# Kernel optimization log

Measured on AMD Instinct MI355X. Metric: run time of the kernel, lower is better.

The kernel has to match this reference:

```python
import jax, jax.numpy as jnp
import numpy as np

DELTA_V = 0.1
DELTA_D = 0.5
NUM_LABELS = 33  # label 0 = background, instance ids 1..32


def setup_inputs() -> dict:
    key = jax.random.key(0)
    k1, k2 = jax.random.split(key)
    B, N, D = 8, 131072, 32
    embeddings = jax.random.normal(k1, (B, N, D), dtype=jnp.float32)
    labels = jax.random.randint(k2, (B, N), 0, NUM_LABELS, dtype=jnp.int32)
    return {"embeddings": embeddings, "labels": labels}


def reference(embeddings, labels):
    # embeddings: [B, N, D], labels: [B, N] int (0 = ignore)
    B = embeddings.shape[0]
    dt = embeddings.dtype

    oh = jax.nn.one_hot(labels, NUM_LABELS, dtype=dt)              # [B, N, L]
    counts = oh.sum(1)                                              # [B, L]
    sums = jnp.einsum('bnl,bnd->bld', oh, embeddings)               # [B, L, D]
    means = sums / jnp.maximum(counts, 1.0)[..., None]              # [B, L, D]

    # ---- pull loss: hinge on distance of each point to its instance mean ----
    mean_pt = jnp.take_along_axis(means, labels[..., None], axis=1)  # [B, N, D]
    diff = embeddings - mean_pt
    dist = jnp.sqrt(jnp.sum(diff * diff, -1) + 1e-24)               # [B, N]
    hinge = jnp.maximum(dist - DELTA_V, 0.0)
    seg_mean = jnp.einsum('bnl,bn->bl', oh, hinge) / jnp.maximum(counts, 1.0)  # [B, L]

    present = counts[:, 1:] > 0                                     # [B, L-1]
    n_inst = present.sum(-1).astype(dt)                             # [B]
    pull_b = seg_mean[:, 1:].sum(-1) / (n_inst + 1e-6)
    pull = pull_b.sum() / B

    # ---- push loss: hinge margin between normalized instance means ----
    m = means[:, 1:, :]                                             # [B, L-1, D]
    mn = m / jnp.maximum(jnp.linalg.norm(m, axis=-1, keepdims=True), 1e-12)
    sq = jnp.sum((mn[:, :, None, :] - mn[:, None, :, :]) ** 2, -1)  # [B, K, K]
    dmat = jnp.sqrt(sq + 1e-24)
    K = NUM_LABELS - 1
    triu = jnp.triu(jnp.ones((K, K), dt), 1)
    pmask = triu[None] * present[:, :, None].astype(dt) * present[:, None, :].astype(dt)
    hp = jnp.maximum(2.0 * DELTA_D - dmat, 0.0) * pmask
    push_b = jnp.where(n_inst > 1, hp.sum((-2, -1)) / (pmask.sum((-2, -1)) + 1e-6), 0.0)
    push = push_b.sum() / B

    total = pull + push
    return jnp.stack([total, pull, push])
```

## Files before the change

### kernel.cpp

```cpp
#include <hip/hip_runtime.h>
#include <hip/hip_bf16.h>

#define BATCH 8
#define NPTS  131072
#define DIM   32
#define NLAB  33
#define G1X   128
#define P1PTS 1024
#define BPB2  128

#define OFF_CNT   0
#define OFF_SUM   264
#define OFF_PULL  (264 + 8448)
#define OFF_PSUM  (OFF_PULL + BATCH * BPB2)
#define OFF_PCNT  (OFF_PSUM + BATCH * G1X * NLAB * DIM)
#define WS_FLOATS (OFF_PCNT + BATCH * G1X * NLAB)

typedef short  bf16x8 __attribute__((ext_vector_type(8)));
typedef float  f32x4  __attribute__((ext_vector_type(4)));
typedef float  f32x2  __attribute__((ext_vector_type(2)));
typedef int    i32x4  __attribute__((ext_vector_type(4)));

static __device__ __forceinline__ short f2bf(float f) {
  __hip_bfloat16 h = __float2bfloat16(f);
  return *reinterpret_cast<short*>(&h);
}

#define P1_WAIT(N)                                                            \
  asm volatile("s_waitcnt vmcnt(" #N ")" ::: "memory");                       \
  __builtin_amdgcn_sched_barrier(0);

#define P1_ISSUE(EV, L0, L1, T)                                               \
  {                                                                           \
    const int vt  = ve + (T) * 4096;                                          \
    const int vlt = vl + (T) * 128;                                           \
    asm volatile("global_load_dwordx4 %0, %1, %2"             : "=&v"(EV[0]) : "v"(vt),  "s"(ebase)); \
    asm volatile("global_load_dwordx4 %0, %1, %2 offset:1024" : "=&v"(EV[1]) : "v"(vt),  "s"(ebase)); \
    asm volatile("global_load_dwordx4 %0, %1, %2 offset:2048" : "=&v"(EV[2]) : "v"(vt),  "s"(ebase)); \
    asm volatile("global_load_dwordx4 %0, %1, %2 offset:3072" : "=&v"(EV[3]) : "v"(vt),  "s"(ebase)); \
    asm volatile("global_load_dwordx4 %0, %1, %2"             : "=&v"(L0)    : "v"(vlt), "s"(lbase)); \
    asm volatile("global_load_dwordx4 %0, %1, %2 offset:16"   : "=&v"(L1)    : "v"(vlt), "s"(lbase)); \
  }

#define P1_STAGE(EV, BUF)                                                     \
  {                                                                           \
    float* st_ = s_st[w][BUF];                                                \
    _Pragma("unroll")                                                         \
    for (int r = 0; r < 4; ++r) {                                             \
      const int idx = (r * 8 + (lane >> 3)) * 34 + (lane & 7) * 4;            \
      *(f32x2*)&st_[idx]     = (f32x2){EV[r][0], EV[r][1]};                   \
      *(f32x2*)&st_[idx + 2] = (f32x2){EV[r][2], EV[r][3]};                   \
    }                                                                         \
  }

#define P1_FRAGA(L0, L1)                                                      \
  {                                                                           \
    _Pragma("unroll")                                                         \
    for (int j = 0; j < 8; ++j) {                                             \
      const int lj = (j < 4) ? L0[j] : L1[j - 4];                             \
      const int h0 = (lj == m0), h1 = (lj == m0 + 16), h2 = (lj == m0 + 32);  \
      a0[j] = h0 ? (short)0x3F80 : (short)0;                                  \
      a1[j] = h1 ? (short)0x3F80 : (short)0;                                  \
      a2[j] = h2 ? (short)0x3F80 : (short)0;                                  \
      cnt0 += h0; cnt1 += h1; cnt2 += h2;                                     \
    }                                                                         \
  }

#define P1_BMFMA(BUF)                                                         \
  {                                                                           \
    const float* st_ = s_st[w][BUF];                                          \
    bf16x8 b0, b1;                                                            \
    _Pragma("unroll")                                                         \
    for (int j = 0; j < 8; ++j) {                                             \
      b0[j] = f2bf(st_[(g * 8 + j) * 34 + m0]);                               \
      b1[j] = f2bf(st_[(g * 8 + j) * 34 + m0 + 16]);                          \
    }                                                                         \
    acc[0][0] = __builtin_amdgcn_mfma_f32_16x16x32_bf16(a0, b0, acc[0][0], 0, 0, 0); \
    acc[0][1] = __builtin_amdgcn_mfma_f32_16x16x32_bf16(a0, b1, acc[0][1], 0, 0, 0); \
    acc[1][0] = __builtin_amdgcn_mfma_f32_16x16x32_bf16(a1, b0, acc[1][0], 0, 0, 0); \
    acc[1][1] = __builtin_amdgcn_mfma_f32_16x16x32_bf16(a1, b1, acc[1][1], 0, 0, 0); \
    acc[2][0] = __builtin_amdgcn_mfma_f32_16x16x32_bf16(a2, b0, acc[2][0], 0, 0, 0); \
    acc[2][1] = __builtin_amdgcn_mfma_f32_16x16x32_bf16(a2, b1, acc[2][1], 0, 0, 0); \
  }

__global__ __launch_bounds__(256) void pass1_kernel(
    const float* __restrict__ emb, const int* __restrict__ lab,
    float* __restrict__ psum, float* __restrict__ pcnt) {
  const int b    = blockIdx.y;
  const int tid  = threadIdx.x;
  const int w    = __builtin_amdgcn_readfirstlane(tid >> 6);
  const int lane = tid & 63;
  const int m0   = lane & 15;
  const int g    = lane >> 4;

  __shared__ float s_st[4][2][1088];
  __shared__ int   s_cnt4[4][NLAB];

  const size_t base = (size_t)b * NPTS + (size_t)blockIdx.x * P1PTS
                    + (size_t)w * 256;
  const float* ebase = emb + base * DIM;
  const int*   lbase = lab + base;
  const int ve = (lane >> 3) * 128 + (lane & 7) * 16;
  const int vl = g * 32;

  f32x4 acc[3][2];
#pragma unroll
  for (int t = 0; t < 3; ++t)
#pragma unroll
    for (int u = 0; u < 2; ++u) acc[t][u] = (f32x4){0.f, 0.f, 0.f, 0.f};
  int cnt0 = 0, cnt1 = 0, cnt2 = 0;
  bf16x8 a0, a1, a2;

  f32x4 eA[4], eB[4];
  i32x4 lA0, lA1, lB0, lB1;

  P1_ISSUE(eA, lA0, lA1, 0);
  P1_ISSUE(eB, lB0, lB1, 1);

  P1_WAIT(6); P1_STAGE(eA, 0); P1_FRAGA(lA0, lA1); P1_ISSUE(eA, lA0, lA1, 2); P1_BMFMA(0);
  P1_WAIT(6); P1_STAGE(eB, 1); P1_FRAGA(lB0, lB1); P1_ISSUE(eB, lB0, lB1, 3); P1_BMFMA(1);
  P1_WAIT(6); P1_STAGE(eA, 0); P1_FRAGA(lA0, lA1); P1_ISSUE(eA, lA0, lA1, 4); P1_BMFMA(0);
  P1_WAIT(6); P1_STAGE(eB, 1); P1_FRAGA(lB0, lB1); P1_ISSUE(eB, lB0, lB1, 5); P1_BMFMA(1);
  P1_WAIT(6); P1_STAGE(eA, 0); P1_FRAGA(lA0, lA1); P1_ISSUE(eA, lA0, lA1, 6); P1_BMFMA(0);
  P1_WAIT(6); P1_STAGE(eB, 1); P1_FRAGA(lB0, lB1); P1_ISSUE(eB, lB0, lB1, 7); P1_BMFMA(1);
  P1_WAIT(6); P1_STAGE(eA, 0); P1_FRAGA(lA0, lA1); P1_BMFMA(0);
  P1_WAIT(0); P1_STAGE(eB, 1); P1_FRAGA(lB0, lB1); P1_BMFMA(1);

  cnt0 += __shfl_xor(cnt0, 16); cnt0 += __shfl_xor(cnt0, 32);
  cnt1 += __shfl_xor(cnt1, 16); cnt1 += __shfl_xor(cnt1, 32);
  cnt2 += __shfl_xor(cnt2, 16); cnt2 += __shfl_xor(cnt2, 32);
  if (lane < 16)            s_cnt4[w][m0]      = cnt0;
  else if (lane < 32)       s_cnt4[w][m0 + 16] = cnt1;
  if (lane == 32)           s_cnt4[w][32]      = cnt2;

  float* st = &s_st[w][0][0];
#pragma unroll
  for (int t = 0; t < 2; ++t)
#pragma unroll
    for (int u = 0; u < 2; ++u)
#pragma unroll
      for (int r = 0; r < 4; ++r)
        st[(t * 16 + g * 4 + r) * DIM + m0 + 16 * u] = acc[t][u][r];
  if (lane < 16) {
    st[32 * DIM + m0]      = acc[2][0][0];
    st[32 * DIM + m0 + 16] = acc[2][1][0];
  }
  __syncthreads();

  const size_t pb = (size_t)b * G1X + blockIdx.x;
  for (int i = tid; i < NLAB * DIM; i += 256) {
    const float v = s_st[0][0][i] + s_st[1][0][i] + s_st[2][0][i] + s_st[3][0][i];
    psum[pb * (NLAB * DIM) + i] = v;
  }
  if (tid < NLAB) {
    const int c = s_cnt4[0][tid] + s_cnt4[1][tid] + s_cnt4[2][tid] + s_cnt4[3][tid];
    pcnt[pb * NLAB + tid] = (float)c;
  }
}

__global__ __launch_bounds__(256) void reduce_kernel(
    const float* __restrict__ psum, const float* __restrict__ pcnt,
    float* __restrict__ gsum, float* __restrict__ gcnt) {
  constexpr int TOT = BATCH * NLAB * DIM;
  constexpr int KS  = G1X / 8;
  const int slice = blockIdx.y;
  const int o = blockIdx.x * 256 + threadIdx.x;
  if (o < TOT) {
    const int b = o / (NLAB * DIM), i = o - b * (NLAB * DIM);
    const float* src = psum + ((size_t)b * G1X + slice * KS) * (NLAB * DIM) + i;
    float a0 = 0.f, a1 = 0.f, a2 = 0.f, a3 = 0.f;
#pragma unroll
    for (int k = 0; k < KS; k += 4) {
      a0 += src[(size_t)(k + 0) * (NLAB * DIM)];
      a1 += src[(size_t)(k + 1) * (NLAB * DIM)];
      a2 += src[(size_t)(k + 2) * (NLAB * DIM)];
      a3 += src[(size_t)(k + 3) * (NLAB * DIM)];
    }
    atomicAdd(&gsum[o], (a0 + a1) + (a2 + a3));
  } else if (o - TOT < BATCH * NLAB) {
    const int o2 = o - TOT;
    const int b = o2 / NLAB, l = o2 - b * NLAB;
    const float* src = pcnt + ((size_t)b * G1X + slice * KS) * NLAB + l;
    float a = 0.f;
#pragma unroll
    for (int k = 0; k < KS; ++k) a += src[(size_t)k * NLAB];
    atomicAdd(&gcnt[o2], a);
  }
}

#define CN 8
#define P2_ISSUE(LB, EB, C)                                                   \
  {                                                                           \
    _Pragma("unroll")                                                         \
    for (int j = 0; j < CN; ++j) {                                            \
      const size_t it = (size_t)(C) * CN + j;                                 \
      const unsigned long long al =                                           \
          (unsigned long long)(lab + base + p0 + it * PSTRIDE);               \
      asm volatile("global_load_dword %0, %1, off" : "=&v"(LB[j]) : "v"(al)); \
    }                                                                         \
    _Pragma("unroll")                                                         \
    for (int j = 0; j < CN; ++j) {                                            \
      const size_t it = (size_t)(C) * CN + j;                                 \
      const unsigned long long ae =                                           \
          (unsigned long long)(emb + (base + p0 + it * PSTRIDE) * DIM + d0);  \
      asm volatile("global_load_dwordx4 %0, %1, off" : "=&v"(EB[j]) : "v"(ae)); \
    }                                                                         \
  }

#define P2_COMPUTE(LB, EB)                                                    \
  {                                                                           \
    float s[CN];                                                              \
    _Pragma("unroll")                                                         \
    for (int j = 0; j < CN; ++j) {                                            \
      const f32x4 mv = *(const f32x4*)(s_mean + LB[j] * 36 + d0);             \
      const float dx = EB[j][0] - mv[0], dy = EB[j][1] - mv[1];               \
      const float dz = EB[j][2] - mv[2], dw = EB[j][3] - mv[3];               \
      s[j] = dx * dx + dy * dy + dz * dz + dw * dw;                           \
    }                                                                         \
    _Pragma("unroll")                                                         \
    for (int j = 0; j < CN; ++j) {                                            \
      s[j] += __shfl_xor(s[j], 1);                                            \
      s[j] += __shfl_xor(s[j], 2);                                            \
      s[j] += __shfl_xor(s[j], 4);                                            \
    }                                                                         \
    float sv = s[0];                                                          \
    int   lv = LB[0];                                                         \
    _Pragma("unroll")                                                         \
    for (int j = 1; j < CN; ++j) {                                            \
      sv = (lane8 == j) ? s[j] : sv;                                          \
      lv = (lane8 == j) ? LB[j] : lv;                                         \
    }                                                                         \
    const float dist = sqrtf(sv + 1e-24f);                                    \
    wacc += s_w[lv] * fmaxf(dist - 0.1f, 0.f);                                \
  }

__global__ __launch_bounds__(256, 4) void pass2_kernel(
    const float* __restrict__ emb, const int* __restrict__ lab,
    const float* __restrict__ gsum, const float* __restrict__ gcnt,
    float* __restrict__ pull_part) {
  const int b   = blockIdx.y;
  const int tid = threadIdx.x;
  __shared__ __align__(16) float s_mean[NLAB * 36];
  __shared__ float s_w[NLAB];
  __shared__ float s_red[4];

  for (int i = tid; i < NLAB * DIM; i += 256) {
    const int l = i >> 5, d = i & 31;
    const float c = gcnt[b * NLAB + l];
    s_mean[l * 36 + d] = gsum[b * (NLAB * DIM) + i] / fmaxf(c, 1.0f);
  }
  if (tid < 64) {
    const float c = (tid < NLAB) ? gcnt[b * NLAB + tid] : 0.f;
    const int pres = (tid >= 1 && tid < NLAB && c > 0.f) ? 1 : 0;
    const unsigned long long bal = __ballot(pres);
    const float n_inst = (float)__popcll(bal);
    if (tid < NLAB)
      s_w[tid] = pres ? 1.f / (fmaxf(c, 1.f) * (n_inst + 1e-6f)) : 0.f;
  }
  __syncthreads();

  const int sub   = tid >> 3;
  const int lane8 = tid & 7;
  const int d0    = lane8 << 2;
  const size_t base = (size_t)b * NPTS;
  const int p0 = blockIdx.x * 32 + sub;
  constexpr int PSTRIDE = BPB2 * 32;
  constexpr int NIT     = NPTS / PSTRIDE;
  constexpr int NCH     = NIT / CN;

  int   labsA[CN], labsB[CN];
  f32x4 eA[CN], eB[CN];
  float wacc = 0.f;

  P2_ISSUE(labsA, eA, 0);
#pragma unroll
  for (int cc = 0; cc < NCH; cc += 2) {
    if (cc + 1 < NCH) P2_ISSUE(labsB, eB, cc + 1);
    if (cc + 1 < NCH) { asm volatile("s_waitcnt vmcnt(16)" ::: "memory"); }
    else              { asm volatile("s_waitcnt vmcnt(0)"  ::: "memory"); }
    __builtin_amdgcn_sched_barrier(0);
    P2_COMPUTE(labsA, eA);
    if (cc + 1 < NCH) {
      if (cc + 2 < NCH) P2_ISSUE(labsA, eA, cc + 2);
      if (cc + 2 < NCH) { asm volatile("s_waitcnt vmcnt(16)" ::: "memory"); }
      else              { asm volatile("s_waitcnt vmcnt(0)"  ::: "memory"); }
      __builtin_amdgcn_sched_barrier(0);
      P2_COMPUTE(labsB, eB);
    }
  }

#pragma unroll
  for (int mm = 1; mm < 64; mm <<= 1) wacc += __shfl_xor(wacc, mm);
  if ((tid & 63) == 0) s_red[tid >> 6] = wacc;
  __syncthreads();
  if (tid == 0)
    pull_part[b * BPB2 + blockIdx.x] =
        s_red[0] + s_red[1] + s_red[2] + s_red[3];
}

__global__ __launch_bounds__(512) void finish_kernel(
    const float* __restrict__ gsum, const float* __restrict__ gcnt,
    const float* __restrict__ pull_part, float* __restrict__ out) {
  const int tid = threadIdx.x;
  const int b   = tid >> 6;
  const int t   = tid & 63;
  __shared__ __align__(16) float s_mn[BATCH * 32 * DIM];
  __shared__ float s_ps[BATCH];
  __shared__ float s_pl[BATCH];
  float* mn = s_mn + b * 32 * DIM;

  {
    float plsum = pull_part[b * BPB2 + t] + pull_part[b * BPB2 + 64 + t];
#pragma unroll
    for (int m = 1; m < 64; m <<= 1) plsum += __shfl_xor(plsum, m);
    if (t == 0) s_pl[b] = plsum;
  }

  int pres = 0;
  if (t < 32) {
    const int l = t + 1;
    const float cnt = gcnt[b * NLAB + l];
    pres = (cnt > 0.f) ? 1 : 0;
    const float inv = 1.f / fmaxf(cnt, 1.f);
    float v[DIM];
    float n2 = 0.f;
    for (int d = 0; d < DIM; d++) {
      v[d] = gsum[b * (NLAB * DIM) + l * DIM + d] * inv;
      n2  += v[d] * v[d];
    }
    const float scale = 1.f / fmaxf(sqrtf(n2), 1e-12f);
    for (int d = 0; d < DIM; d++) mn[t * DIM + d] = v[d] * scale;
  }
  const unsigned long long bal = __ballot(pres);
  const unsigned int pmask32 = (unsigned int)(bal & 0xFFFFFFFFull);
  const int n_inst = __popc(pmask32);

  __syncthreads();

  float hp_sum = 0.f, pm_sum = 0.f;
  for (int idx = t; idx < 1024; idx += 64) {
    const int i = idx >> 5, j = idx & 31;
    if (j > i && ((pmask32 >> i) & 1u) && ((pmask32 >> j) & 1u)) {
      const float4* a = (const float4*)(mn + i * DIM);
      const float4* c = (const float4*)(mn + j * DIM);
      float sq = 0.f;
      for (int q = 0; q < 8; q++) {
        const float4 av = a[q], cv = c[q];
        const float dx = av.x - cv.x, dy = av.y - cv.y;
        const float dz = av.z - cv.z, dw = av.w - cv.w;
        sq += dx * dx + dy * dy + dz * dz + dw * dw;
      }
      const float dmat = sqrtf(sq + 1e-24f);
      hp_sum += fmaxf(1.0f - dmat, 0.f);
      pm_sum += 1.f;
    }
  }
  for (int m = 1; m < 64; m <<= 1) {
    hp_sum += __shfl_xor(hp_sum, m);
    pm_sum += __shfl_xor(pm_sum, m);
  }
  const float push = (n_inst > 1) ? hp_sum / (pm_sum + 1e-6f) : 0.f;
  if (t == 0) s_ps[b] = push;
  __syncthreads();

  if (tid < 64) {
    float pl = (t < BATCH) ? s_pl[t] : 0.f;
    float ps = (t < BATCH) ? s_ps[t] : 0.f;
#pragma unroll
    for (int m = 1; m < 64; m <<= 1) {
      pl += __shfl_xor(pl, m);
      ps += __shfl_xor(ps, m);
    }
    if (t == 0) {
      const float pull_m = pl / (float)BATCH;
      const float push_m = ps / (float)BATCH;
      out[0] = pull_m + push_m;
      out[1] = pull_m;
      out[2] = push_m;
    }
  }
}

extern "C" void kernel_launch(void* const* d_in, const int* in_sizes, int n_in,
                              void* d_out, int out_size, void* d_ws, size_t ws_size,
                              hipStream_t stream) {
  const float* emb = (const float*)d_in[0];
  const int*   lab = (const int*)d_in[1];
  float* out = (float*)d_out;
  float* ws  = (float*)d_ws;

  float* gcnt  = ws + OFF_CNT;
  float* gsum  = ws + OFF_SUM;
  float* pullp = ws + OFF_PULL;
  float* psum  = ws + OFF_PSUM;
  float* pcnt  = ws + OFF_PCNT;

  hipMemsetAsync(d_ws, 0, (OFF_SUM + BATCH * NLAB * DIM) * sizeof(float), stream);

  dim3 grid1(G1X, BATCH);
  dim3 gridR((BATCH * NLAB * DIM + BATCH * NLAB + 255) / 256, 8);
  dim3 grid2(BPB2, BATCH);
  pass1_kernel<<<grid1, 256, 0, stream>>>(emb, lab, psum, pcnt);
  reduce_kernel<<<gridR, 256, 0, stream>>>(psum, pcnt, gsum, gcnt);
  pass2_kernel<<<grid2, 256, 0, stream>>>(emb, lab, gsum, gcnt, pullp);
  finish_kernel<<<1, 512, 0, stream>>>(gsum, gcnt, pullp, out);
}
```

Before: 233.8 us.

## Fold reduce and finish kernels into last-block-done tails of pass1 and pass2

Removes the separate reduce and finish kernel launches. Each pass1 block now bumps a per-batch atomic counter, and the last block for that batch reduces all partial sums and counts into gsum/gcnt. The last pass2 block across the grid computes the push loss and the final output. This saves two launches and their gaps, and the memset shrinks to a few counters. The cost is that the cross-block reduction is serialized onto one block per batch, which relies on threadfence/atomic ordering.

```diff
diff --git a/kernel.cpp b/kernel.cpp
--- a/kernel.cpp
+++ b/kernel.cpp
@@ -12,7 +12,8 @@
 #define OFF_CNT   0
 #define OFF_SUM   264
 #define OFF_PULL  (264 + 8448)
-#define OFF_PSUM  (OFF_PULL + BATCH * BPB2)
+#define OFF_DCNT  (OFF_PULL + BATCH * BPB2)
+#define OFF_PSUM  (OFF_DCNT + 16)
 #define OFF_PCNT  (OFF_PSUM + BATCH * G1X * NLAB * DIM)
 #define WS_FLOATS (OFF_PCNT + BATCH * G1X * NLAB)
 
@@ -85,7 +86,9 @@
 
 __global__ __launch_bounds__(256) void pass1_kernel(
     const float* __restrict__ emb, const int* __restrict__ lab,
-    float* __restrict__ psum, float* __restrict__ pcnt) {
+    float* __restrict__ psum, float* __restrict__ pcnt,
+    float* __restrict__ gsum, float* __restrict__ gcnt,
+    unsigned* __restrict__ dcnt) {
   const int b    = blockIdx.y;
   const int tid  = threadIdx.x;
   const int w    = __builtin_amdgcn_readfirstlane(tid >> 6);
@@ -95,6 +98,7 @@
 
   __shared__ float s_st[4][2][1088];
   __shared__ int   s_cnt4[4][NLAB];
+  __shared__ unsigned s_old;
 
   const size_t base = (size_t)b * NPTS + (size_t)blockIdx.x * P1PTS
                     + (size_t)w * 256;
@@ -156,35 +160,31 @@
     const int c = s_cnt4[0][tid] + s_cnt4[1][tid] + s_cnt4[2][tid] + s_cnt4[3][tid];
     pcnt[pb * NLAB + tid] = (float)c;
   }
-}
-
-__global__ __launch_bounds__(256) void reduce_kernel(
-    const float* __restrict__ psum, const float* __restrict__ pcnt,
-    float* __restrict__ gsum, float* __restrict__ gcnt) {
-  constexpr int TOT = BATCH * NLAB * DIM;
-  constexpr int KS  = G1X / 8;
-  const int slice = blockIdx.y;
-  const int o = blockIdx.x * 256 + threadIdx.x;
-  if (o < TOT) {
-    const int b = o / (NLAB * DIM), i = o - b * (NLAB * DIM);
-    const float* src = psum + ((size_t)b * G1X + slice * KS) * (NLAB * DIM) + i;
-    float a0 = 0.f, a1 = 0.f, a2 = 0.f, a3 = 0.f;
-#pragma unroll
-    for (int k = 0; k < KS; k += 4) {
-      a0 += src[(size_t)(k + 0) * (NLAB * DIM)];
-      a1 += src[(size_t)(k + 1) * (NLAB * DIM)];
-      a2 += src[(size_t)(k + 2) * (NLAB * DIM)];
-      a3 += src[(size_t)(k + 3) * (NLAB * DIM)];
+
+  __threadfence();
+  __syncthreads();
+  if (tid == 0) s_old = atomicAdd(&dcnt[b], 1u);
+  __syncthreads();
+  if (s_old == G1X - 1) {
+    for (int i = tid; i < NLAB * DIM; i += 256) {
+      const float* src = psum + (size_t)b * G1X * (NLAB * DIM) + i;
+      float r0 = 0.f, r1 = 0.f, r2 = 0.f, r3 = 0.f;
+#pragma unroll 4
+      for (int k = 0; k < G1X; k += 4) {
+        r0 += src[(size_t)(k + 0) * (NLAB * DIM)];
+        r1 += src[(size_t)(k + 1) * (NLAB * DIM)];
+        r2 += src[(size_t)(k + 2) * (NLAB * DIM)];
+        r3 += src[(size_t)(k + 3) * (NLAB * DIM)];
+      }
+      gsum[b * (NLAB * DIM) + i] = (r0 + r1) + (r2 + r3);
     }
-    atomicAdd(&gsum[o], (a0 + a1) + (a2 + a3));
-  } else if (o - TOT < BATCH * NLAB) {
-    const int o2 = o - TOT;
-    const int b = o2 / NLAB, l = o2 - b * NLAB;
-    const float* src = pcnt + ((size_t)b * G1X + slice * KS) * NLAB + l;
-    float a = 0.f;
-#pragma unroll
-    for (int k = 0; k < KS; ++k) a += src[(size_t)k * NLAB];
-    atomicAdd(&gcnt[o2], a);
+    for (int l = tid; l < NLAB; l += 256) {
+      const float* src = pcnt + (size_t)b * G1X * NLAB + l;
+      float r = 0.f;
+#pragma unroll 4
+      for (int k = 0; k < G1X; ++k) r += src[(size_t)k * NLAB];
+      gcnt[b * NLAB + l] = r;
+    }
   }
 }
 
@@ -237,12 +237,16 @@
 __global__ __launch_bounds__(256, 4) void pass2_kernel(
     const float* __restrict__ emb, const int* __restrict__ lab,
     const float* __restrict__ gsum, const float* __restrict__ gcnt,
-    float* __restrict__ pull_part) {
+    float* __restrict__ pull_part, unsigned* __restrict__ dcnt,
+    float* __restrict__ out) {
   const int b   = blockIdx.y;
   const int tid = threadIdx.x;
   __shared__ __align__(16) float s_mean[NLAB * 36];
   __shared__ float s_w[NLAB];
   __shared__ float s_red[4];
+  __shared__ __align__(16) float s_fin[4][32][36];
+  __shared__ float s_out[BATCH][2];
+  __shared__ unsigned s_old2;
 
   for (int i = tid; i < NLAB * DIM; i += 256) {
     const int l = i >> 5, d = i & 31;
@@ -296,87 +300,83 @@
   if (tid == 0)
     pull_part[b * BPB2 + blockIdx.x] =
         s_red[0] + s_red[1] + s_red[2] + s_red[3];
-}
-
-__global__ __launch_bounds__(512) void finish_kernel(
-    const float* __restrict__ gsum, const float* __restrict__ gcnt,
-    const float* __restrict__ pull_part, float* __restrict__ out) {
-  const int tid = threadIdx.x;
-  const int b   = tid >> 6;
-  const int t   = tid & 63;
-  __shared__ __align__(16) float s_mn[BATCH * 32 * DIM];
-  __shared__ float s_ps[BATCH];
-  __shared__ float s_pl[BATCH];
-  float* mn = s_mn + b * 32 * DIM;
-
-  {
-    float plsum = pull_part[b * BPB2 + t] + pull_part[b * BPB2 + 64 + t];
-#pragma unroll
-    for (int m = 1; m < 64; m <<= 1) plsum += __shfl_xor(plsum, m);
-    if (t == 0) s_pl[b] = plsum;
-  }
-
-  int pres = 0;
-  if (t < 32) {
-    const int l = t + 1;
-    const float cnt = gcnt[b * NLAB + l];
-    pres = (cnt > 0.f) ? 1 : 0;
-    const float inv = 1.f / fmaxf(cnt, 1.f);
-    float v[DIM];
-    float n2 = 0.f;
-    for (int d = 0; d < DIM; d++) {
-      v[d] = gsum[b * (NLAB * DIM) + l * DIM + d] * inv;
-      n2  += v[d] * v[d];
+
+  __threadfence();
+  __syncthreads();
+  if (tid == 0) s_old2 = atomicAdd(&dcnt[8], 1u);
+  __syncthreads();
+  if (s_old2 == BPB2 * BATCH - 1) {
+    const int wv = tid >> 6, t = tid & 63;
+    for (int bb = wv; bb < BATCH; bb += 4) {
+      float pl = pull_part[bb * BPB2 + t] + pull_part[bb * BPB2 + 64 + t];
+#pragma unroll
+      for (int m = 1; m < 64; m <<= 1) pl += __shfl_xor(pl, m);
+
+      int pres = 0;
+      if (t < 32) {
+        const int l = t + 1;
+        const float cnt = gcnt[bb * NLAB + l];
+        pres = (cnt > 0.f) ? 1 : 0;
+        const float inv = 1.f / fmaxf(cnt, 1.f);
+        float v[DIM];
+        float n2 = 0.f;
+        for (int d = 0; d < DIM; d++) {
+          v[d] = gsum[bb * (NLAB * DIM) + l * DIM + d] * inv;
+          n2  += v[d] * v[d];
+        }
+        const float sc = 1.f / fmaxf(sqrtf(n2), 1e-12f);
+        for (int d = 0; d < DIM; d++) s_fin[wv][t][d] = v[d] * sc;
+      }
+      const unsigned long long bal = __ballot(pres);
+      const unsigned pm32 = (unsigned)(bal & 0xFFFFFFFFull);
+      const int n_inst = __popc(pm32);
+      asm volatile("s_waitcnt lgkmcnt(0)" ::: "memory");
+      __builtin_amdgcn_sched_barrier(0);
+
+      float hp = 0.f, pm = 0.f;
+      for (int idx = t; idx < 1024; idx += 64) {
+        const int i = idx >> 5, j = idx & 31;
+        if (j > i && ((pm32 >> i) & 1u) && ((pm32 >> j) & 1u)) {
+          const float4* a = (const float4*)&s_fin[wv][i][0];
+          const float4* c = (const float4*)&s_fin[wv][j][0];
+          float sq = 0.f;
+          for (int q = 0; q < 8; q++) {
+            const float4 av = a[q], cv = c[q];
+            const float dx = av.x - cv.x, dy = av.y - cv.y;
+            const float dz = av.z - cv.z, dw = av.w - cv.w;
+            sq += dx * dx + dy * dy + dz * dz + dw * dw;
+          }
+          const float dm = sqrtf(sq + 1e-24f);
+          hp += fmaxf(1.0f - dm, 0.f);
+          pm += 1.f;
+        }
+      }
+#pragma unroll
+      for (int m = 1; m < 64; m <<= 1) {
+        hp += __shfl_xor(hp, m);
+        pm += __shfl_xor(pm, m);
+      }
+      if (t == 0) {
+        s_out[bb][0] = pl;
+        s_out[bb][1] = (n_inst > 1) ? hp / (pm + 1e-6f) : 0.f;
+      }
     }
-    const float scale = 1.f / fmaxf(sqrtf(n2), 1e-12f);
-    for (int d = 0; d < DIM; d++) mn[t * DIM + d] = v[d] * scale;
-  }
-  const unsigned long long bal = __ballot(pres);
-  const unsigned int pmask32 = (unsigned int)(bal & 0xFFFFFFFFull);
-  const int n_inst = __popc(pmask32);
-
-  __syncthreads();
-
-  float hp_sum = 0.f, pm_sum = 0.f;
-  for (int idx = t; idx < 1024; idx += 64) {
-    const int i = idx >> 5, j = idx & 31;
-    if (j > i && ((pmask32 >> i) & 1u) && ((pmask32 >> j) & 1u)) {
-      const float4* a = (const float4*)(mn + i * DIM);
-      const float4* c = (const float4*)(mn + j * DIM);
-      float sq = 0.f;
-      for (int q = 0; q < 8; q++) {
-        const float4 av = a[q], cv = c[q];
-        const float dx = av.x - cv.x, dy = av.y - cv.y;
-        const float dz = av.z - cv.z, dw = av.w - cv.w;
-        sq += dx * dx + dy * dy + dz * dz + dw * dw;
-      }
-      const float dmat = sqrtf(sq + 1e-24f);
-      hp_sum += fmaxf(1.0f - dmat, 0.f);
-      pm_sum += 1.f;
-    }
-  }
-  for (int m = 1; m < 64; m <<= 1) {
-    hp_sum += __shfl_xor(hp_sum, m);
-    pm_sum += __shfl_xor(pm_sum, m);
-  }
-  const float push = (n_inst > 1) ? hp_sum / (pm_sum + 1e-6f) : 0.f;
-  if (t == 0) s_ps[b] = push;
-  __syncthreads();
-
-  if (tid < 64) {
-    float pl = (t < BATCH) ? s_pl[t] : 0.f;
-    float ps = (t < BATCH) ? s_ps[t] : 0.f;
-#pragma unroll
-    for (int m = 1; m < 64; m <<= 1) {
-      pl += __shfl_xor(pl, m);
-      ps += __shfl_xor(ps, m);
-    }
-    if (t == 0) {
-      const float pull_m = pl / (float)BATCH;
-      const float push_m = ps / (float)BATCH;
-      out[0] = pull_m + push_m;
-      out[1] = pull_m;
-      out[2] = push_m;
+    __syncthreads();
+    if (tid < 64) {
+      float pl = (tid < BATCH) ? s_out[tid][0] : 0.f;
+      float ps = (tid < BATCH) ? s_out[tid][1] : 0.f;
+#pragma unroll
+      for (int m = 1; m < 64; m <<= 1) {
+        pl += __shfl_xor(pl, m);
+        ps += __shfl_xor(ps, m);
+      }
+      if (tid == 0) {
+        const float pull_m = pl / (float)BATCH;
+        const float push_m = ps / (float)BATCH;
+        out[0] = pull_m + push_m;
+        out[1] = pull_m;
+        out[2] = push_m;
+      }
     }
   }
 }
@@ -389,19 +389,18 @@
   float* out = (float*)d_out;
   float* ws  = (float*)d_ws;
 
-  float* gcnt  = ws + OFF_CNT;
-  float* gsum  = ws + OFF_SUM;
-  float* pullp = ws + OFF_PULL;
-  float* psum  = ws + OFF_PSUM;
-  float* pcnt  = ws + OFF_PCNT;
-
-  hipMemsetAsync(d_ws, 0, (OFF_SUM + BATCH * NLAB * DIM) * sizeof(float), stream);
+  float*    gcnt  = ws + OFF_CNT;
+  float*    gsum  = ws + OFF_SUM;
+  float*    pullp = ws + OFF_PULL;
+  unsigned* dcnt  = (unsigned*)(ws + OFF_DCNT);
+  float*    psum  = ws + OFF_PSUM;
+  float*    pcnt  = ws + OFF_PCNT;
+
+  hipMemsetAsync((char*)d_ws + OFF_DCNT * sizeof(float), 0,
+                 16 * sizeof(unsigned), stream);
 
   dim3 grid1(G1X, BATCH);
-  dim3 gridR((BATCH * NLAB * DIM + BATCH * NLAB + 255) / 256, 8);
   dim3 grid2(BPB2, BATCH);
-  pass1_kernel<<<grid1, 256, 0, stream>>>(emb, lab, psum, pcnt);
-  reduce_kernel<<<gridR, 256, 0, stream>>>(psum, pcnt, gsum, gcnt);
-  pass2_kernel<<<grid2, 256, 0, stream>>>(emb, lab, gsum, gcnt, pullp);
-  finish_kernel<<<1, 512, 0, stream>>>(gsum, gcnt, pullp, out);
+  pass1_kernel<<<grid1, 256, 0, stream>>>(emb, lab, psum, pcnt, gsum, gcnt, dcnt);
+  pass2_kernel<<<grid2, 256, 0, stream>>>(emb, lab, gsum, gcnt, pullp, dcnt, out);
 }
```

Result: slower. 563.5 us (+141.0%).
